# Kernel tuning notes

Measured on AMD Instinct MI355X. Metric: run time of the kernel, lower is better.

Reference implementation:

```python
import jax, jax.numpy as jnp
import numpy as np

N_NODES = 100000
N_EDGES = 3200000
IN_CH = 128
HID = 128
N_GRAPHS = 128
BN_EPS = 1e-5


def _gcn_conv(x, W, b, src, dst, n_nodes):
    # x: [N, Cin] -> [N, Cout]; PyG GCNConv: linear, add self-loops,
    # symmetric D^-1/2 A D^-1/2 normalization, scatter-add at dst, + bias.
    xw = x @ W  # [N, Cout]
    loop = jnp.arange(n_nodes, dtype=src.dtype)
    s = jnp.concatenate([src, loop])
    d = jnp.concatenate([dst, loop])
    deg = jax.ops.segment_sum(jnp.ones_like(d, dtype=xw.dtype), d, num_segments=n_nodes)
    dinv = jnp.where(deg > 0, jax.lax.rsqrt(deg), 0.0)
    coef = (dinv[s] * dinv[d])[:, None]  # [E+N, 1]
    msg = xw[s] * coef  # gather + scale
    out = jax.ops.segment_sum(msg, d, num_segments=n_nodes)  # scatter-add
    return out + b


def setup_inputs() -> dict:
    key = jax.random.key(0)
    ks = jax.random.split(key, 8)
    x = jax.random.normal(ks[0], (N_NODES, IN_CH), dtype=jnp.float32)
    edge_index = jax.random.randint(ks[1], (2, N_EDGES), 0, N_NODES, dtype=jnp.int64)
    batch = jnp.sort(jax.random.randint(ks[2], (N_NODES,), 0, N_GRAPHS, dtype=jnp.int64))
    W1 = jax.random.normal(ks[3], (IN_CH, HID), dtype=jnp.float32) / np.sqrt(IN_CH)
    W2 = jax.random.normal(ks[4], (HID, HID), dtype=jnp.float32) / np.sqrt(HID)
    fw1 = jax.random.normal(ks[5], (HID, HID // 2), dtype=jnp.float32) / np.sqrt(HID)
    cw = jax.random.normal(ks[6], (HID // 2, 2), dtype=jnp.float32) / np.sqrt(HID // 2)
    return {
        "x": x,
        "edge_index": edge_index,
        "batch": batch,
        "W1": W1,
        "b1": jnp.zeros((HID,), jnp.float32),
        "gamma": jnp.ones((HID,), jnp.float32),
        "beta": jnp.zeros((HID,), jnp.float32),
        "rmean": jnp.zeros((HID,), jnp.float32),
        "rvar": jnp.ones((HID,), jnp.float32),
        "W2": W2,
        "b2": jnp.zeros((HID,), jnp.float32),
        "fw1": fw1,
        "fb1": jnp.zeros((HID // 2,), jnp.float32),
        "cw": cw,
        "cb": jnp.zeros((2,), jnp.float32),
    }


def reference(x, edge_index, batch, W1, b1, gamma, beta, rmean, rvar, W2, b2, fw1, fb1, cw, cb):
    src, dst = edge_index[0], edge_index[1]
    h = _gcn_conv(x, W1, b1, src, dst, N_NODES)
    # BatchNorm1d in inference mode (running stats); dropout is identity in eval.
    h = (h - rmean) * jax.lax.rsqrt(rvar + BN_EPS) * gamma + beta
    h = jax.nn.relu(h)
    h = _gcn_conv(h, W2, b2, src, dst, N_NODES)
    # global_mean_pool over graphs
    sums = jax.ops.segment_sum(h, batch, num_segments=N_GRAPHS)  # [G, H]
    cnts = jax.ops.segment_sum(jnp.ones((N_NODES,), h.dtype), batch, num_segments=N_GRAPHS)
    pooled = sums / jnp.maximum(cnts, 1.0)[:, None]
    z = jax.nn.relu(pooled @ fw1 + fb1)
    return z @ cw + cb
```

## Files before the change

kernel.cpp:

```cpp
#include <hip/hip_runtime.h>
#include <hip/hip_bf16.h>

#define N_NODES 100000
#define N_EDGES 3200000
#define CH 128
#define NG 128
#define BN_EPS 1e-5f
#define NBUCK 1024
#define BCAP 4096
#define EPB 8192
#define NBINB 391
#define BPAD 32
#define NSPB 1563

using i32x4 = __attribute__((ext_vector_type(4))) int;

__device__ __forceinline__ unsigned int packq(const float* v, float inv) {
    int q0 = __float2int_rn(v[0] * inv), q1 = __float2int_rn(v[1] * inv);
    int q2 = __float2int_rn(v[2] * inv), q3 = __float2int_rn(v[3] * inv);
    return (unsigned int)(q0 & 255) | ((unsigned int)(q1 & 255) << 8) |
           ((unsigned int)(q2 & 255) << 16) | ((unsigned int)(q3 & 255) << 24);
}

__global__ __launch_bounds__(256) void k_bin(
    const int* __restrict__ src, const int* __restrict__ dst,
    int* __restrict__ bcur, unsigned int* __restrict__ pairs,
    const float* __restrict__ W1, const float* __restrict__ W2,
    const float* __restrict__ gamma, const float* __restrict__ beta,
    const float* __restrict__ rmean, const float* __restrict__ rvar, const float* __restrict__ b1,
    unsigned char* __restrict__ Wq1T, float* __restrict__ wcs1,
    unsigned char* __restrict__ Wq2T, float* __restrict__ wcs2,
    float* __restrict__ A1, float* __restrict__ B1) {
    int t = threadIdx.x;
    if (blockIdx.x == NBINB) {
        const float* W = (t < 128) ? W1 : W2;
        unsigned char* WT = (t < 128) ? Wq1T : Wq2T;
        float* wcs = (t < 128) ? wcs1 : wcs2;
        int c = t & 127;
        float m = 0.f;
        for (int k = 0; k < 128; ++k) m = fmaxf(m, fabsf(W[k * CH + c]));
        float inv = (m > 0.f) ? 127.0f / m : 0.f;
        for (int k = 0; k < 128; ++k) {
            int q = __float2int_rn(W[k * CH + c] * inv);
            WT[c * CH + k] = (unsigned char)(q & 255);
        }
        wcs[c] = m * (1.0f / 127.0f);
        if (t < 128) {
            float a = gamma[c] * rsqrtf(rvar[c] + BN_EPS);
            A1[c] = a;
            B1[c] = (b1[c] - rmean[c]) * a + beta[c];
        }
        return;
    }
    __shared__ int lhist[NBUCK];
    __shared__ int lbase[NBUCK];
    for (int i = t; i < NBUCK; i += 256) lhist[i] = 0;
    __syncthreads();
    int base = blockIdx.x * EPB;
    int lim = min(base + EPB, N_EDGES);
    for (int e = base + t; e < lim; e += 256)
        atomicAdd(&lhist[dst[e] >> 7], 1);
    __syncthreads();
    for (int i = t; i < NBUCK; i += 256) {
        int h = lhist[i];
        lbase[i] = h ? ((i << 12) + atomicAdd(&bcur[i * BPAD], h)) : 0;
        lhist[i] = 0;
    }
    __syncthreads();
    for (int e = base + t; e < lim; e += 256) {
        int d = dst[e];
        int b = d >> 7;
        int r = atomicAdd(&lhist[b], 1);
        pairs[lbase[b] + r] = ((unsigned int)src[e] << 7) | ((unsigned int)d & 127u);
    }
}

__global__ __launch_bounds__(256) void k_bfill(const unsigned int* __restrict__ pairs,
                                               const int* __restrict__ bcur,
                                               int* __restrict__ offs, int* __restrict__ deg,
                                               float* __restrict__ dinv, int* __restrict__ perm) {
    __shared__ int lcur[1024];
    __shared__ int loff[1024];
    __shared__ int sm[256];
    int b = blockIdx.x;
    int t = threadIdx.x;
    for (int i = t; i < 1024; i += 256) lcur[i] = 0;
    __syncthreads();
    int p0 = b << 12;
    int p1 = p0 + bcur[b * BPAD];
    for (int p = p0 + t; p < p1; p += 256) {
        unsigned int e = pairs[p];
        int idx = (int)((e & 127u) << 3) | (int)((e >> 7) >> 14);
        atomicAdd(&lcur[idx], 1);
    }
    __syncthreads();
    int4 v = *(const int4*)&lcur[t * 4];
    int tsum = v.x + v.y + v.z + v.w;
    sm[t] = tsum;
    __syncthreads();
    for (int off = 1; off < 256; off <<= 1) {
        int val = sm[t];
        int add = (t >= off) ? sm[t - off] : 0;
        __syncthreads();
        sm[t] = val + add;
        __syncthreads();
    }
    int excl = sm[t] - tsum + p0;
    loff[t * 4]     = excl;
    loff[t * 4 + 1] = excl + v.x;
    loff[t * 4 + 2] = excl + v.x + v.y;
    loff[t * 4 + 3] = excl + v.x + v.y + v.z;
    lcur[t * 4] = 0; lcur[t * 4 + 1] = 0; lcur[t * 4 + 2] = 0; lcur[t * 4 + 3] = 0;
    __syncthreads();
    if (t < 128) {
        int node = (b << 7) + t;
        if (node < N_NODES) {
            int o0 = loff[t * 8];
            int o1 = (t == 127) ? p1 : loff[(t + 1) * 8];
            int cnt = o1 - o0;
            offs[node] = o0;
            deg[node] = cnt;
            dinv[node] = rsqrtf((float)(cnt + 1));
        }
    }
    __syncthreads();
    for (int p = p0 + t; p < p1; p += 256) {
        unsigned int e = pairs[p];
        int srcn = (int)(e >> 7);
        int idx = (int)((e & 127u) << 3) | (srcn >> 14);
        int r = atomicAdd(&lcur[idx], 1);
        perm[loff[idx] + r] = srcn;
    }
}

__global__ __launch_bounds__(256) void k_gemm_f32(
    const float* __restrict__ X,
    const unsigned char* __restrict__ WT, const float* __restrict__ wcs,
    const float* __restrict__ dinvp, unsigned char* __restrict__ Yq, float* __restrict__ ospre) {
    __shared__ float ep[4][16][132];
    int t = threadIdx.x;
    int w = t >> 6;
    int lane = t & 63;
    int quad = lane >> 4, l16 = lane & 15;
    int row0 = blockIdx.x * 64 + w * 16;

    int arow = row0 + l16;
    if (arow >= N_NODES) arow = N_NODES - 1;

    float xv[32];
    {
        const float4* p0 = (const float4*)&X[(size_t)arow * CH + quad * 16];
        const float4* p1 = (const float4*)&X[(size_t)arow * CH + 64 + quad * 16];
        #pragma unroll
        for (int q = 0; q < 4; ++q) {
            float4 f = p0[q];
            xv[q * 4 + 0] = f.x; xv[q * 4 + 1] = f.y; xv[q * 4 + 2] = f.z; xv[q * 4 + 3] = f.w;
        }
        #pragma unroll
        for (int q = 0; q < 4; ++q) {
            float4 f = p1[q];
            xv[16 + q * 4 + 0] = f.x; xv[16 + q * 4 + 1] = f.y;
            xv[16 + q * 4 + 2] = f.z; xv[16 + q * 4 + 3] = f.w;
        }
    }
    float m = 0.f;
    #pragma unroll
    for (int j = 0; j < 32; ++j) m = fmaxf(m, fabsf(xv[j]));
    m = fmaxf(m, __shfl_xor(m, 16, 64));
    m = fmaxf(m, __shfl_xor(m, 32, 64));
    float inv = (m > 0.f) ? 127.0f / m : 0.f;
    float ms = m * (1.0f / 127.0f);
    unsigned int pk[8];
    #pragma unroll
    for (int j = 0; j < 8; ++j) pk[j] = packq(&xv[j * 4], inv);
    i32x4 a0 = (i32x4){(int)pk[0], (int)pk[1], (int)pk[2], (int)pk[3]};
    i32x4 a1 = (i32x4){(int)pk[4], (int)pk[5], (int)pk[6], (int)pk[7]};

    i32x4 acc[8];
    #pragma unroll
    for (int i = 0; i < 8; ++i) acc[i] = (i32x4){0, 0, 0, 0};
    #pragma unroll
    for (int tt = 0; tt < 8; ++tt) {
        int n = tt * 16 + l16;
        i32x4 b0 = *(const i32x4*)&WT[(size_t)n * CH + quad * 16];
        i32x4 b1 = *(const i32x4*)&WT[(size_t)n * CH + 64 + quad * 16];
        acc[tt] = __builtin_amdgcn_mfma_i32_16x16x64_i8(a0, b0, acc[tt], 0, 0, 0);
        acc[tt] = __builtin_amdgcn_mfma_i32_16x16x64_i8(a1, b1, acc[tt], 0, 0, 0);
    }

    float xsr[4];
    #pragma unroll
    for (int r = 0; r < 4; ++r) xsr[r] = __shfl(ms, quad * 4 + r, 64);
    #pragma unroll
    for (int tt = 0; tt < 8; ++tt) {
        float wc = wcs[tt * 16 + l16];
        #pragma unroll
        for (int r = 0; r < 4; ++r)
            ep[w][quad * 4 + r][tt * 16 + l16] = (float)acc[tt][r] * xsr[r] * wc;
    }
    __syncthreads();

    int rl = lane >> 2, part = lane & 3;
    int grow = row0 + rl;
    float v[32];
    float mm = 0.f;
    #pragma unroll
    for (int i = 0; i < 32; ++i) {
        v[i] = ep[w][rl][part * 32 + i];
        mm = fmaxf(mm, fabsf(v[i]));
    }
    mm = fmaxf(mm, __shfl_xor(mm, 1, 64));
    mm = fmaxf(mm, __shfl_xor(mm, 2, 64));
    if (grow < N_NODES) {
        float inv2 = (mm > 0.f) ? 127.0f / mm : 0.f;
        unsigned int o[8];
        #pragma unroll
        for (int q = 0; q < 8; ++q) o[q] = packq(&v[q * 4], inv2);
        uint4* dst0 = (uint4*)&Yq[(size_t)grow * CH + part * 32];
        dst0[0] = make_uint4(o[0], o[1], o[2], o[3]);
        dst0[1] = make_uint4(o[4], o[5], o[6], o[7]);
        if (part == 0) ospre[grow] = (mm * (1.0f / 127.0f)) * dinvp[grow];
    }
}

__global__ __launch_bounds__(256) void k_gemm_mfma(
    const unsigned char* __restrict__ Xq, const float* __restrict__ xs,
    const unsigned char* __restrict__ WT, const float* __restrict__ wcs,
    const float* __restrict__ dinvp, unsigned char* __restrict__ Yq, float* __restrict__ ospre) {
    __shared__ float ep[4][16][132];
    int t = threadIdx.x;
    int w = t >> 6;
    int lane = t & 63;
    int quad = lane >> 4, l16 = lane & 15;
    int row0 = blockIdx.x * 64 + w * 16;

    int arow = row0 + l16;
    if (arow >= N_NODES) arow = N_NODES - 1;
    i32x4 a0 = *(const i32x4*)&Xq[(size_t)arow * CH + quad * 16];
    i32x4 a1 = *(const i32x4*)&Xq[(size_t)arow * CH + 64 + quad * 16];

    i32x4 acc[8];
    #pragma unroll
    for (int i = 0; i < 8; ++i) acc[i] = (i32x4){0, 0, 0, 0};

    #pragma unroll
    for (int tt = 0; tt < 8; ++tt) {
        int n = tt * 16 + l16;
        i32x4 b0 = *(const i32x4*)&WT[(size_t)n * CH + quad * 16];
        i32x4 b1 = *(const i32x4*)&WT[(size_t)n * CH + 64 + quad * 16];
        acc[tt] = __builtin_amdgcn_mfma_i32_16x16x64_i8(a0, b0, acc[tt], 0, 0, 0);
        acc[tt] = __builtin_amdgcn_mfma_i32_16x16x64_i8(a1, b1, acc[tt], 0, 0, 0);
    }

    float xsr[4];
    #pragma unroll
    for (int r = 0; r < 4; ++r) {
        int rr = row0 + quad * 4 + r;
        xsr[r] = xs[(rr < N_NODES) ? rr : (N_NODES - 1)];
    }
    #pragma unroll
    for (int tt = 0; tt < 8; ++tt) {
        float wc = wcs[tt * 16 + l16];
        #pragma unroll
        for (int r = 0; r < 4; ++r)
            ep[w][quad * 4 + r][tt * 16 + l16] = (float)acc[tt][r] * xsr[r] * wc;
    }
    __syncthreads();

    int rl = lane >> 2, part = lane & 3;
    int grow = row0 + rl;
    float v[32];
    float m = 0.f;
    #pragma unroll
    for (int i = 0; i < 32; ++i) {
        v[i] = ep[w][rl][part * 32 + i];
        m = fmaxf(m, fabsf(v[i]));
    }
    m = fmaxf(m, __shfl_xor(m, 1, 64));
    m = fmaxf(m, __shfl_xor(m, 2, 64));
    if (grow < N_NODES) {
        float inv = (m > 0.f) ? 127.0f / m : 0.f;
        unsigned int o[8];
        #pragma unroll
        for (int q = 0; q < 8; ++q) o[q] = packq(&v[q * 4], inv);
        uint4* dst0 = (uint4*)&Yq[(size_t)grow * CH + part * 32];
        dst0[0] = make_uint4(o[0], o[1], o[2], o[3]);
        dst0[1] = make_uint4(o[4], o[5], o[6], o[7]);
        if (part == 0) ospre[grow] = (m * (1.0f / 127.0f)) * dinvp[grow];
    }
}

#define ACCI8(f, v)                                                                    \
    { int _a = (int)v.x, _b = (int)v.y;                                                \
      acc[0] += f * (float)((_a << 24) >> 24);                                         \
      acc[1] += f * (float)((_a << 16) >> 24);                                         \
      acc[2] += f * (float)((_a << 8) >> 24);                                          \
      acc[3] += f * (float)(_a >> 24);                                                 \
      acc[4] += f * (float)((_b << 24) >> 24);                                         \
      acc[5] += f * (float)((_b << 16) >> 24);                                         \
      acc[6] += f * (float)((_b << 8) >> 24);                                          \
      acc[7] += f * (float)(_b >> 24); }

#define SPMM_ROW_GATHER()                                                              \
    float di = 0.f; int beg = 0, end = 0;                                              \
    if (valid) { di = dinv[row]; beg = offs[row]; end = beg + deg[row]; }              \
    float acc[8];                                                                      \
    _Pragma("unroll") for (int j = 0; j < 8; ++j) acc[j] = 0.f;                        \
    for (int cb = beg; cb < end; cb += 8) {                                            \
        int k0 = cb + g, k1 = cb + g + 4;                                              \
        int ka0 = (k0 < end) ? k0 : (end - 1);                                         \
        int ka1 = (k1 < end) ? k1 : (end - 1);                                         \
        int s0 = perm[ka0], s1 = perm[ka1];                                            \
        float f0 = (k0 < end) ? di : 0.f;                                              \
        float f1 = (k1 < end) ? di : 0.f;                                              \
        f0 *= spre[s0]; f1 *= spre[s1];                                                \
        uint2 v0 = xq[(size_t)s0 * 16 + c];                                            \
        uint2 v1 = xq[(size_t)s1 * 16 + c];                                            \
        ACCI8(f0, v0) ACCI8(f1, v1)                                                    \
    }                                                                                  \
    _Pragma("unroll") for (int j = 0; j < 8; ++j) {                                    \
        acc[j] += __shfl_xor(acc[j], 16, 64);                                          \
        acc[j] += __shfl_xor(acc[j], 32, 64);                                          \
    }

__global__ __launch_bounds__(256) void k_spmm_bn_relu(
    const uint2* __restrict__ xq, const int* __restrict__ perm, const int* __restrict__ offs,
    const int* __restrict__ deg, const float* __restrict__ dinv, const float* __restrict__ spre,
    const float* __restrict__ A1, const float* __restrict__ B1,
    uint2* __restrict__ outq, float* __restrict__ osraw) {
    int w = threadIdx.x >> 6;
    int lane = threadIdx.x & 63;
    int g = lane >> 4, c = lane & 15;
    int base = blockIdx.x * 64;
    for (int i = 0; i < 16; ++i) {
        int row = __builtin_amdgcn_readfirstlane(base + i * 4 + w);
        bool valid = row < N_NODES;
        SPMM_ROW_GATHER()
        if (g == 0 && valid) {
            uint2 v = xq[(size_t)row * 16 + c];
            float fs = di * spre[row];
            ACCI8(fs, v)
            int ch = c * 8;
            float r[8];
            const float4* A4 = (const float4*)&A1[ch];
            const float4* B4 = (const float4*)&B1[ch];
            #pragma unroll
            for (int q = 0; q < 2; ++q) {
                float4 aa = A4[q], bb = B4[q];
                r[q * 4 + 0] = fmaxf(acc[q * 4 + 0] * aa.x + bb.x, 0.f);
                r[q * 4 + 1] = fmaxf(acc[q * 4 + 1] * aa.y + bb.y, 0.f);
                r[q * 4 + 2] = fmaxf(acc[q * 4 + 2] * aa.z + bb.z, 0.f);
                r[q * 4 + 3] = fmaxf(acc[q * 4 + 3] * aa.w + bb.w, 0.f);
            }
            float m = 0.f;
            #pragma unroll
            for (int j = 0; j < 8; ++j) m = fmaxf(m, r[j]);
            #pragma unroll
            for (int off = 1; off < 16; off <<= 1) m = fmaxf(m, __shfl_xor(m, off, 64));
            float inv = (m > 0.f) ? 127.0f / m : 0.f;
            uint2 pk;
            pk.x = packq(&r[0], inv);
            pk.y = packq(&r[4], inv);
            outq[(size_t)row * 16 + c] = pk;
            if (c == 0) osraw[row] = m * (1.0f / 127.0f);
        }
    }
}

__global__ __launch_bounds__(256) void k_spmm_pool(
    const uint2* __restrict__ xq, const int* __restrict__ perm, const int* __restrict__ offs,
    const int* __restrict__ deg, const float* __restrict__ dinv, const float* __restrict__ spre,
    const float* __restrict__ bias, const int* __restrict__ batch,
    float* __restrict__ psum, int* __restrict__ pcnt) {
    __shared__ float red[4][128];
    __shared__ int gid[4];
    int w = threadIdx.x >> 6;
    int lane = threadIdx.x & 63;
    int g = lane >> 4, c = lane & 15;
    int base = blockIdx.x * 64;
    for (int i = 0; i < 16; ++i) {
        int row = __builtin_amdgcn_readfirstlane(base + i * 4 + w);
        bool valid = row < N_NODES;
        SPMM_ROW_GATHER()
        if (g == 0) {
            int ch = c * 8;
            if (valid) {
                uint2 v = xq[(size_t)row * 16 + c];
                float fs = di * spre[row];
                ACCI8(fs, v)
                #pragma unroll
                for (int j = 0; j < 8; ++j) red[w][ch + j] = acc[j] + bias[ch + j];
            } else {
                #pragma unroll
                for (int j = 0; j < 8; ++j) red[w][ch + j] = 0.f;
            }
        }
        if (lane == 0) gid[w] = valid ? batch[row] : -1;
        __syncthreads();
        bool same = (gid[0] >= 0) && (gid[0] == gid[1]) && (gid[1] == gid[2]) && (gid[2] == gid[3]);
        int c0 = lane * 2;
        if (same) {
            if (w == 0) {
                float sx = red[0][c0] + red[1][c0] + red[2][c0] + red[3][c0];
                float sy = red[0][c0 + 1] + red[1][c0 + 1] + red[2][c0 + 1] + red[3][c0 + 1];
                unsafeAtomicAdd(&psum[gid[0] * CH + c0], sx);
                unsafeAtomicAdd(&psum[gid[0] * CH + c0 + 1], sy);
                if (lane == 0) atomicAdd(&pcnt[gid[0]], 4);
            }
        } else if (gid[w] >= 0) {
            unsafeAtomicAdd(&psum[gid[w] * CH + c0], red[w][c0]);
            unsafeAtomicAdd(&psum[gid[w] * CH + c0 + 1], red[w][c0 + 1]);
            if (lane == 0) atomicAdd(&pcnt[gid[w]], 1);
        }
        __syncthreads();
    }
}

__global__ __launch_bounds__(128) void k_head(const float* __restrict__ psum, const int* __restrict__ pcnt,
                                              const float* __restrict__ fw1, const float* __restrict__ fb1,
                                              const float* __restrict__ cw, const float* __restrict__ cb,
                                              float* __restrict__ out) {
    __shared__ float fws[128 * 64];
    for (int i = threadIdx.x; i < 128 * 64; i += 128) fws[i] = fw1[i];
    __syncthreads();
    int g = threadIdx.x;
    float z[64];
    #pragma unroll
    for (int j = 0; j < 64; ++j) z[j] = fb1[j];
    float cnt = fmaxf((float)pcnt[g], 1.f);
    float inv = 1.f / cnt;
    for (int c = 0; c < 128; ++c) {
        float p = psum[g * CH + c] * inv;
        #pragma unroll
        for (int j = 0; j < 64; ++j) z[j] += p * fws[c * 64 + j];
    }
    float o0 = cb[0], o1 = cb[1];
    #pragma unroll
    for (int j = 0; j < 64; ++j) {
        float zz = fmaxf(z[j], 0.f);
        o0 += zz * cw[j * 2];
        o1 += zz * cw[j * 2 + 1];
    }
    out[g * 2] = o0;
    out[g * 2 + 1] = o1;
}

extern "C" void kernel_launch(void* const* d_in, const int* in_sizes, int n_in,
                              void* d_out, int out_size, void* d_ws, size_t ws_size,
                              hipStream_t stream) {
    const float* x     = (const float*)d_in[0];
    const int*   ei    = (const int*)d_in[1];
    const int*   batch = (const int*)d_in[2];
    const float* W1    = (const float*)d_in[3];
    const float* b1    = (const float*)d_in[4];
    const float* gamma = (const float*)d_in[5];
    const float* beta  = (const float*)d_in[6];
    const float* rmean = (const float*)d_in[7];
    const float* rvar  = (const float*)d_in[8];
    const float* W2    = (const float*)d_in[9];
    const float* b2    = (const float*)d_in[10];
    const float* fw1   = (const float*)d_in[11];
    const float* fb1   = (const float*)d_in[12];
    const float* cw    = (const float*)d_in[13];
    const float* cb    = (const float*)d_in[14];
    const int* srcp = ei;
    const int* dstp = ei + N_EDGES;

    char* w = (char*)d_ws;
    int*   bcur  = (int*)w;   w += NBUCK * BPAD * 4;
    float* psum  = (float*)w; w += 65536;
    int*   pcnt  = (int*)w;   w += 512;
    size_t zbytes = (size_t)NBUCK * BPAD * 4 + 65536 + 512;
    int*   deg   = (int*)w;   w += 400000;
    int*   offs  = (int*)w;   w += 400000;
    float* dinv  = (float*)w; w += 400000;
    float* spreA = (float*)w; w += 400000;
    float* srawB = (float*)w; w += 400000;
    float* spreC = (float*)w; w += 400000;
    float* A1    = (float*)w; w += 512;
    float* B1    = (float*)w; w += 512;
    float* wcs1  = (float*)w; w += 512;
    float* wcs2  = (float*)w; w += 512;
    unsigned char* Wq1T = (unsigned char*)w; w += 16384;
    unsigned char* Wq2T = (unsigned char*)w; w += 16384;
    unsigned int* pairs = (unsigned int*)w; w += (size_t)NBUCK * BCAP * 4;
    int*   perm  = (int*)w;   w += (size_t)NBUCK * BCAP * 4;
    unsigned char* bufA = (unsigned char*)w; w += 12800000;
    unsigned char* bufB = (unsigned char*)w; w += 12800000;
    unsigned char* bufC = (unsigned char*)w; w += 12800000;

    hipMemsetAsync(d_ws, 0, zbytes, stream);
    k_bin<<<NBINB + 1, 256, 0, stream>>>(srcp, dstp, bcur, pairs,
                                         W1, W2, gamma, beta, rmean, rvar, b1,
                                         Wq1T, wcs1, Wq2T, wcs2, A1, B1);
    k_bfill<<<NBUCK, 256, 0, stream>>>(pairs, bcur, offs, deg, dinv, perm);
    k_gemm_f32<<<1563, 256, 0, stream>>>(x, Wq1T, wcs1, dinv, bufA, spreA);
    k_spmm_bn_relu<<<NSPB, 256, 0, stream>>>((const uint2*)bufA, perm, offs, deg, dinv, spreA,
                                             A1, B1, (uint2*)bufB, srawB);
    k_gemm_mfma<<<1563, 256, 0, stream>>>(bufB, srawB, Wq2T, wcs2, dinv, bufC, spreC);
    k_spmm_pool<<<NSPB, 256, 0, stream>>>((const uint2*)bufC, perm, offs, deg, dinv, spreC,
                                          b2, batch, psum, pcnt);
    k_head<<<1, 128, 0, stream>>>(psum, pcnt, fw1, fb1, cw, cb, (float*)d_out);
}
```

Baseline: 463.9 us.

## Reorder second GCN layer to aggregate before applying W2, fusing GEMM into pooling

The second GCN layer now aggregates the quantized BN/ReLU output first and applies W2 afterwards, using the identity A(XW) = (AX)W. The separate int8 MFMA GEMM kernel, its intermediate buffer and the W2 quantization are removed. The pooling kernel now does a per-row 128x128 fp32 matvec with shuffle reductions before accumulating into graph sums. This cuts one kernel launch and a full pass over a 12.8MB buffer, but adds substantial per-row FMA and shuffle work inside the gather kernel.

```diff
diff --git a/kernel.cpp b/kernel.cpp
--- a/kernel.cpp
+++ b/kernel.cpp
@@ -25,27 +25,23 @@
 __global__ __launch_bounds__(256) void k_bin(
     const int* __restrict__ src, const int* __restrict__ dst,
     int* __restrict__ bcur, unsigned int* __restrict__ pairs,
-    const float* __restrict__ W1, const float* __restrict__ W2,
+    const float* __restrict__ W1,
     const float* __restrict__ gamma, const float* __restrict__ beta,
     const float* __restrict__ rmean, const float* __restrict__ rvar, const float* __restrict__ b1,
     unsigned char* __restrict__ Wq1T, float* __restrict__ wcs1,
-    unsigned char* __restrict__ Wq2T, float* __restrict__ wcs2,
     float* __restrict__ A1, float* __restrict__ B1) {
     int t = threadIdx.x;
     if (blockIdx.x == NBINB) {
-        const float* W = (t < 128) ? W1 : W2;
-        unsigned char* WT = (t < 128) ? Wq1T : Wq2T;
-        float* wcs = (t < 128) ? wcs1 : wcs2;
-        int c = t & 127;
-        float m = 0.f;
-        for (int k = 0; k < 128; ++k) m = fmaxf(m, fabsf(W[k * CH + c]));
-        float inv = (m > 0.f) ? 127.0f / m : 0.f;
-        for (int k = 0; k < 128; ++k) {
-            int q = __float2int_rn(W[k * CH + c] * inv);
-            WT[c * CH + k] = (unsigned char)(q & 255);
-        }
-        wcs[c] = m * (1.0f / 127.0f);
         if (t < 128) {
+            int c = t;
+            float m = 0.f;
+            for (int k = 0; k < 128; ++k) m = fmaxf(m, fabsf(W1[k * CH + c]));
+            float inv = (m > 0.f) ? 127.0f / m : 0.f;
+            for (int k = 0; k < 128; ++k) {
+                int q = __float2int_rn(W1[k * CH + c] * inv);
+                Wq1T[c * CH + k] = (unsigned char)(q & 255);
+            }
+            wcs1[c] = m * (1.0f / 127.0f);
             float a = gamma[c] * rsqrtf(rvar[c] + BN_EPS);
             A1[c] = a;
             B1[c] = (b1[c] - rmean[c]) * a + beta[c];
@@ -223,73 +219,6 @@
     }
 }
 
-__global__ __launch_bounds__(256) void k_gemm_mfma(
-    const unsigned char* __restrict__ Xq, const float* __restrict__ xs,
-    const unsigned char* __restrict__ WT, const float* __restrict__ wcs,
-    const float* __restrict__ dinvp, unsigned char* __restrict__ Yq, float* __restrict__ ospre) {
-    __shared__ float ep[4][16][132];
-    int t = threadIdx.x;
-    int w = t >> 6;
-    int lane = t & 63;
-    int quad = lane >> 4, l16 = lane & 15;
-    int row0 = blockIdx.x * 64 + w * 16;
-
-    int arow = row0 + l16;
-    if (arow >= N_NODES) arow = N_NODES - 1;
-    i32x4 a0 = *(const i32x4*)&Xq[(size_t)arow * CH + quad * 16];
-    i32x4 a1 = *(const i32x4*)&Xq[(size_t)arow * CH + 64 + quad * 16];
-
-    i32x4 acc[8];
-    #pragma unroll
-    for (int i = 0; i < 8; ++i) acc[i] = (i32x4){0, 0, 0, 0};
-
-    #pragma unroll
-    for (int tt = 0; tt < 8; ++tt) {
-        int n = tt * 16 + l16;
-        i32x4 b0 = *(const i32x4*)&WT[(size_t)n * CH + quad * 16];
-        i32x4 b1 = *(const i32x4*)&WT[(size_t)n * CH + 64 + quad * 16];
-        acc[tt] = __builtin_amdgcn_mfma_i32_16x16x64_i8(a0, b0, acc[tt], 0, 0, 0);
-        acc[tt] = __builtin_amdgcn_mfma_i32_16x16x64_i8(a1, b1, acc[tt], 0, 0, 0);
-    }
-
-    float xsr[4];
-    #pragma unroll
-    for (int r = 0; r < 4; ++r) {
-        int rr = row0 + quad * 4 + r;
-        xsr[r] = xs[(rr < N_NODES) ? rr : (N_NODES - 1)];
-    }
-    #pragma unroll
-    for (int tt = 0; tt < 8; ++tt) {
-        float wc = wcs[tt * 16 + l16];
-        #pragma unroll
-        for (int r = 0; r < 4; ++r)
-            ep[w][quad * 4 + r][tt * 16 + l16] = (float)acc[tt][r] * xsr[r] * wc;
-    }
-    __syncthreads();
-
-    int rl = lane >> 2, part = lane & 3;
-    int grow = row0 + rl;
-    float v[32];
-    float m = 0.f;
-    #pragma unroll
-    for (int i = 0; i < 32; ++i) {
-        v[i] = ep[w][rl][part * 32 + i];
-        m = fmaxf(m, fabsf(v[i]));
-    }
-    m = fmaxf(m, __shfl_xor(m, 1, 64));
-    m = fmaxf(m, __shfl_xor(m, 2, 64));
-    if (grow < N_NODES) {
-        float inv = (m > 0.f) ? 127.0f / m : 0.f;
-        unsigned int o[8];
-        #pragma unroll
-        for (int q = 0; q < 8; ++q) o[q] = packq(&v[q * 4], inv);
-        uint4* dst0 = (uint4*)&Yq[(size_t)grow * CH + part * 32];
-        dst0[0] = make_uint4(o[0], o[1], o[2], o[3]);
-        dst0[1] = make_uint4(o[4], o[5], o[6], o[7]);
-        if (part == 0) ospre[grow] = (m * (1.0f / 127.0f)) * dinvp[grow];
-    }
-}
-
 #define ACCI8(f, v)                                                                    \
     { int _a = (int)v.x, _b = (int)v.y;                                                \
       acc[0] += f * (float)((_a << 24) >> 24);                                         \
@@ -301,7 +230,7 @@
       acc[6] += f * (float)((_b << 8) >> 24);                                          \
       acc[7] += f * (float)(_b >> 24); }
 
-#define SPMM_ROW_GATHER()                                                              \
+#define SPMM_GATHER_LOOP()                                                             \
     float di = 0.f; int beg = 0, end = 0;                                              \
     if (valid) { di = dinv[row]; beg = offs[row]; end = beg + deg[row]; }              \
     float acc[8];                                                                      \
@@ -317,7 +246,9 @@
         uint2 v0 = xq[(size_t)s0 * 16 + c];                                            \
         uint2 v1 = xq[(size_t)s1 * 16 + c];                                            \
         ACCI8(f0, v0) ACCI8(f1, v1)                                                    \
-    }                                                                                  \
+    }
+
+#define SPMM_REDUCE()                                                                  \
     _Pragma("unroll") for (int j = 0; j < 8; ++j) {                                    \
         acc[j] += __shfl_xor(acc[j], 16, 64);                                          \
         acc[j] += __shfl_xor(acc[j], 32, 64);                                          \
@@ -327,7 +258,7 @@
     const uint2* __restrict__ xq, const int* __restrict__ perm, const int* __restrict__ offs,
     const int* __restrict__ deg, const float* __restrict__ dinv, const float* __restrict__ spre,
     const float* __restrict__ A1, const float* __restrict__ B1,
-    uint2* __restrict__ outq, float* __restrict__ osraw) {
+    uint2* __restrict__ outq, float* __restrict__ ospreB) {
     int w = threadIdx.x >> 6;
     int lane = threadIdx.x & 63;
     int g = lane >> 4, c = lane & 15;
@@ -335,7 +266,8 @@
     for (int i = 0; i < 16; ++i) {
         int row = __builtin_amdgcn_readfirstlane(base + i * 4 + w);
         bool valid = row < N_NODES;
-        SPMM_ROW_GATHER()
+        SPMM_GATHER_LOOP()
+        SPMM_REDUCE()
         if (g == 0 && valid) {
             uint2 v = xq[(size_t)row * 16 + c];
             float fs = di * spre[row];
@@ -362,7 +294,7 @@
             pk.x = packq(&r[0], inv);
             pk.y = packq(&r[4], inv);
             outq[(size_t)row * 16 + c] = pk;
-            if (c == 0) osraw[row] = m * (1.0f / 127.0f);
+            if (c == 0) ospreB[row] = m * (1.0f / 127.0f) * di;
         }
     }
 }
@@ -370,7 +302,7 @@
 __global__ __launch_bounds__(256) void k_spmm_pool(
     const uint2* __restrict__ xq, const int* __restrict__ perm, const int* __restrict__ offs,
     const int* __restrict__ deg, const float* __restrict__ dinv, const float* __restrict__ spre,
-    const float* __restrict__ bias, const int* __restrict__ batch,
+    const float* __restrict__ W2f, const float* __restrict__ bias, const int* __restrict__ batch,
     float* __restrict__ psum, int* __restrict__ pcnt) {
     __shared__ float red[4][128];
     __shared__ int gid[4];
@@ -381,18 +313,41 @@
     for (int i = 0; i < 16; ++i) {
         int row = __builtin_amdgcn_readfirstlane(base + i * 4 + w);
         bool valid = row < N_NODES;
-        SPMM_ROW_GATHER()
-        if (g == 0) {
-            int ch = c * 8;
-            if (valid) {
-                uint2 v = xq[(size_t)row * 16 + c];
-                float fs = di * spre[row];
-                ACCI8(fs, v)
+        SPMM_GATHER_LOOP()
+        if (g == 0 && valid) {
+            uint2 v = xq[(size_t)row * 16 + c];
+            float fs = di * spre[row];
+            ACCI8(fs, v)
+        }
+        SPMM_REDUCE()
+        #pragma unroll
+        for (int h = 0; h < 2; ++h) {
+            float out[16];
+            #pragma unroll
+            for (int j = 0; j < 16; ++j) out[j] = 0.f;
+            #pragma unroll
+            for (int k = 0; k < 8; ++k) {
+                const float4* wr = (const float4*)&W2f[(size_t)(c * 8 + k) * CH + g * 32 + h * 16];
+                float a = acc[k];
                 #pragma unroll
-                for (int j = 0; j < 8; ++j) red[w][ch + j] = acc[j] + bias[ch + j];
-            } else {
+                for (int q = 0; q < 4; ++q) {
+                    float4 ww = wr[q];
+                    out[q * 4 + 0] += a * ww.x;
+                    out[q * 4 + 1] += a * ww.y;
+                    out[q * 4 + 2] += a * ww.z;
+                    out[q * 4 + 3] += a * ww.w;
+                }
+            }
+            #pragma unroll
+            for (int off = 1; off < 16; off <<= 1) {
                 #pragma unroll
-                for (int j = 0; j < 8; ++j) red[w][ch + j] = 0.f;
+                for (int j = 0; j < 16; ++j) out[j] += __shfl_xor(out[j], off, 64);
+            }
+            if (c == 0) {
+                #pragma unroll
+                for (int j = 0; j < 16; ++j)
+                    red[w][g * 32 + h * 16 + j] =
+                        valid ? (out[j] + bias[g * 32 + h * 16 + j]) : 0.f;
             }
         }
         if (lane == 0) gid[w] = valid ? batch[row] : -1;
@@ -475,30 +430,25 @@
     int*   offs  = (int*)w;   w += 400000;
     float* dinv  = (float*)w; w += 400000;
     float* spreA = (float*)w; w += 400000;
-    float* srawB = (float*)w; w += 400000;
-    float* spreC = (float*)w; w += 400000;
+    float* spreB = (float*)w; w += 400000;
     float* A1    = (float*)w; w += 512;
     float* B1    = (float*)w; w += 512;
     float* wcs1  = (float*)w; w += 512;
-    float* wcs2  = (float*)w; w += 512;
     unsigned char* Wq1T = (unsigned char*)w; w += 16384;
-    unsigned char* Wq2T = (unsigned char*)w; w += 16384;
     unsigned int* pairs = (unsigned int*)w; w += (size_t)NBUCK * BCAP * 4;
     int*   perm  = (int*)w;   w += (size_t)NBUCK * BCAP * 4;
     unsigned char* bufA = (unsigned char*)w; w += 12800000;
     unsigned char* bufB = (unsigned char*)w; w += 12800000;
-    unsigned char* bufC = (unsigned char*)w; w += 12800000;
 
     hipMemsetAsync(d_ws, 0, zbytes, stream);
     k_bin<<<NBINB + 1, 256, 0, stream>>>(srcp, dstp, bcur, pairs,
-                                         W1, W2, gamma, beta, rmean, rvar, b1,
-                                         Wq1T, wcs1, Wq2T, wcs2, A1, B1);
+                                         W1, gamma, beta, rmean, rvar, b1,
+                                         Wq1T, wcs1, A1, B1);
     k_bfill<<<NBUCK, 256, 0, stream>>>(pairs, bcur, offs, deg, dinv, perm);
     k_gemm_f32<<<1563, 256, 0, stream>>>(x, Wq1T, wcs1, dinv, bufA, spreA);
     k_spmm_bn_relu<<<NSPB, 256, 0, stream>>>((const uint2*)bufA, perm, offs, deg, dinv, spreA,
-                                             A1, B1, (uint2*)bufB, srawB);
-    k_gemm_mfma<<<1563, 256, 0, stream>>>(bufB, srawB, Wq2T, wcs2, dinv, bufC, spreC);
-    k_spmm_pool<<<NSPB, 256, 0, stream>>>((const uint2*)bufC, perm, offs, deg, dinv, spreC,
-                                          b2, batch, psum, pcnt);
+                                             A1, B1, (uint2*)bufB, spreB);
+    k_spmm_pool<<<NSPB, 256, 0, stream>>>((const uint2*)bufB, perm, offs, deg, dinv, spreB,
+                                          W2, b2, batch, psum, pcnt);
     k_head<<<1, 128, 0, stream>>>(psum, pcnt, fw1, fb1, cw, cb, (float*)d_out);
 }
```

New measurement: 1.212 ms. 2.61x slower.
